# Kernel optimization log

Measured on AMD Instinct MI355X. Metric: run time of the kernel, lower is better.

## Reference

```python
import jax, jax.numpy as jnp
import numpy as np


def setup_inputs() -> dict:
    key = jax.random.key(0)
    k1, k2, k3, k4, k5 = jax.random.split(key, 5)
    B, S, IC, OC = 4, 2048, 4096, 4096
    n_out = int(0.05 * IC)  # 204 outlier columns
    return {
        "x": jax.random.normal(k1, (B, S, IC), dtype=jnp.float32),
        "weight": jax.random.normal(k2, (OC, IC), dtype=jnp.float32) * 0.02,
        "bias": jax.random.normal(k3, (OC,), dtype=jnp.float32) * 0.02,
        "outlier_weight": jax.random.normal(k4, (OC, n_out), dtype=jnp.float32) * 0.02,
        "outlier_columns_index": jax.random.randint(k5, (n_out,), 0, IC, dtype=jnp.int32),
    }


def reference(x, weight, bias, outlier_weight, outlier_columns_index):
    # XnorBinaryLinear.quant_weight: per-output-row mean-centering,
    # sign binarization, scaled by per-row mean absolute value.
    mean = jnp.mean(weight, axis=1, keepdims=True)            # [OC, 1]
    centered = weight - mean                                  # [OC, IC]
    scale = jnp.mean(jnp.abs(centered), axis=1, keepdims=True)  # [OC, 1]
    q = jnp.sign(centered) * scale                            # binarized weight [OC, IC]
    # scatter fp32 outlier columns back into the binarized weight
    w = q.at[:, outlier_columns_index].set(outlier_weight)    # [OC, IC]
    # F.linear(x, w, bias) = x @ w.T + bias
    out = jnp.einsum('bsi,oi->bso', x, w) + bias
    return out
```

## Files before the change

kernel.cpp:

```cpp
#include <hip/hip_runtime.h>
#include <hip/hip_bf16.h>


typedef __attribute__((ext_vector_type(4))) int i32x4;

__global__ void init_colmap_kernel(int* __restrict__ cm, int IC) {
    int i = blockIdx.x * 256 + threadIdx.x;
    if (i < IC) cm[i] = -1;
}

__global__ void scatter_colmap_kernel(const int* __restrict__ idx,
                                      int* __restrict__ cm, int n) {
    int j = blockIdx.x * 256 + threadIdx.x;
    if (j < n) atomicMax(&cm[idx[j]], j);
}

__global__ void quant_sign_kernel(const float* __restrict__ w,
                                  signed char* __restrict__ qw,
                                  float* __restrict__ sArr,
                                  float* __restrict__ meanArr,
                                  int IC, int K2) {
    __shared__ float red[8];
    const int o = blockIdx.x;
    const int t = threadIdx.x;
    const int lane = t & 63, wid = t >> 6;

    const float4* row4 = (const float4*)(w + (size_t)o * IC);
    float4 v[4];
    float s = 0.f;
#pragma unroll
    for (int j = 0; j < 4; ++j) {
        v[j] = row4[t + j * 256];
        s += v[j].x + v[j].y + v[j].z + v[j].w;
    }
#pragma unroll
    for (int off = 32; off; off >>= 1) s += __shfl_down(s, off);
    if (lane == 0) red[wid] = s;
    __syncthreads();
    const float mean = (red[0] + red[1] + red[2] + red[3]) / (float)IC;

    float a = 0.f;
#pragma unroll
    for (int j = 0; j < 4; ++j)
        a += fabsf(v[j].x - mean) + fabsf(v[j].y - mean) +
             fabsf(v[j].z - mean) + fabsf(v[j].w - mean);
#pragma unroll
    for (int off = 32; off; off >>= 1) a += __shfl_down(a, off);
    if (lane == 0) red[4 + wid] = a;
    __syncthreads();
    const float scale = (red[4] + red[5] + red[6] + red[7]) / (float)IC;

    if (t == 0) { sArr[o] = scale; meanArr[o] = mean; }

    const size_t base = (size_t)o * K2;
#pragma unroll
    for (int j = 0; j < 4; ++j) {
        const int c0 = (t + j * 256) * 4;
        float ee[4] = {v[j].x, v[j].y, v[j].z, v[j].w};
        int pack = 0;
#pragma unroll
        for (int ei = 0; ei < 4; ++ei) {
            float c = ee[ei] - mean;
            int q = c > 0.f ? 8 : (c < 0.f ? -8 : 0);
            pack |= (q & 0xff) << (ei * 8);
        }
        *(int*)(qw + base + c0) = pack;
    }
}

__global__ void corr_w_kernel(const float* __restrict__ w,
                              const float* __restrict__ ow,
                              const int* __restrict__ idx,
                              const int* __restrict__ cm,
                              const float* __restrict__ sArr,
                              const float* __restrict__ meanArr,
                              signed char* __restrict__ qw,
                              int IC, int K2, int n_out) {
    const int o = blockIdx.x;
    const int j = threadIdx.x;
    signed char q = 0;
    if (j < n_out) {
        const int c = idx[j];
        if (cm[c] == j) {
            const float s = sArr[o];
            const float cen = w[(size_t)o * IC + c] - meanArr[o];
            const float sg = cen > 0.f ? 1.f : (cen < 0.f ? -1.f : 0.f);
            const float wc = ow[(size_t)o * n_out + j] - s * sg;
            float qf = rintf(8.f * wc / s);
            qf = fminf(127.f, fmaxf(-127.f, qf));
            q = (signed char)(int)qf;
        }
    }
    qw[(size_t)o * K2 + IC + j] = q;
}

__global__ void quant_x_kernel(const float4* __restrict__ x4,
                               signed char* __restrict__ qx,
                               float* __restrict__ rdel,
                               int IC, int K2) {
    __shared__ float red[4];
    __shared__ float bmax;
    const int m = blockIdx.x;
    const int t = threadIdx.x;
    const int lane = t & 63, wid = t >> 6;

    const float4* row4 = x4 + (size_t)m * (IC / 4);
    float4 v[4];
    float mx = 0.f;
#pragma unroll
    for (int j = 0; j < 4; ++j) {
        v[j] = row4[t + j * 256];
        mx = fmaxf(mx, fmaxf(fmaxf(fabsf(v[j].x), fabsf(v[j].y)),
                             fmaxf(fabsf(v[j].z), fabsf(v[j].w))));
    }
#pragma unroll
    for (int off = 32; off; off >>= 1) mx = fmaxf(mx, __shfl_down(mx, off));
    if (lane == 0) red[wid] = mx;
    __syncthreads();
    if (t == 0) {
        float m0 = fmaxf(fmaxf(red[0], red[1]), fmaxf(red[2], red[3]));
        bmax = m0;
        rdel[m] = m0 / 127.f;
    }
    __syncthreads();
    const float inv = 127.f / bmax;

    const size_t base = (size_t)m * K2;
#pragma unroll
    for (int j = 0; j < 4; ++j) {
        const int c0 = (t + j * 256) * 4;
        float ee[4] = {v[j].x, v[j].y, v[j].z, v[j].w};
        int pack = 0;
#pragma unroll
        for (int ei = 0; ei < 4; ++ei) {
            int q = (int)rintf(ee[ei] * inv);
            pack |= (q & 0xff) << (ei * 8);
        }
        *(int*)(qx + base + c0) = pack;
    }
}

__global__ void gather_xo_kernel(signed char* __restrict__ qx,
                                 const int* __restrict__ idx,
                                 int IC, int K2, int n_out) {
    const int m = blockIdx.x;
    const int j = threadIdx.x;
    signed char v = 0;
    if (j < n_out) v = qx[(size_t)m * K2 + idx[j]];
    qx[(size_t)m * K2 + IC + j] = v;
}

#define GLDS(src, dst) __builtin_amdgcn_global_load_lds( \
    (const __attribute__((address_space(1))) void*)(src), \
    (__attribute__((address_space(3))) void*)(dst), 16, 0, 0)

#define STAGE64(MAT, bufS, knB) do {                                          \
    const signed char* gsrc_ = (MAT) ? Bblk : Ablk;                           \
    _Pragma("unroll")                                                         \
    for (int rr_ = 0; rr_ < 2; ++rr_) {                                       \
      GLDS(gsrc_ + (size_t)(rr_ * 128 + stg_row) * K2 + (knB) + stg_col,      \
           &ldsb[(bufS) * 32768 + (MAT) * 16384 + (rr_ * 128 + wid * 16) * 64]); \
    } } while (0)

#define RDA(AF, FH, B_) do {                                                  \
    const signed char* pa_ = &ldsb[(B_) * 32768];                             \
    _Pragma("unroll")                                                         \
    for (int j_ = 0; j_ < 4; ++j_)                                            \
      AF[j_] = *(const i32x4*)&pa_[(wr * 128 + ((FH) * 4 + j_) * 16 + l15) * 64 + slB]; \
  } while (0)

#define RDB(BF, B_) do {                                                      \
    const signed char* pb_ = &ldsb[(B_) * 32768 + 16384];                     \
    _Pragma("unroll")                                                         \
    for (int j_ = 0; j_ < 4; ++j_)                                            \
      BF[j_] = *(const i32x4*)&pb_[(wc * 64 + j_ * 16 + l15) * 64 + slB];     \
  } while (0)

#define MM16(FH) do {                                                         \
    _Pragma("unroll")                                                         \
    for (int mi_ = 0; mi_ < 4; ++mi_)                                         \
      _Pragma("unroll")                                                       \
      for (int ni_ = 0; ni_ < 4; ++ni_)                                       \
        acc[(FH) * 4 + mi_][ni_] = __builtin_amdgcn_mfma_i32_16x16x64_i8(     \
            afr[mi_], bfr[ni_], acc[(FH) * 4 + mi_][ni_], 0, 0, 0);           \
  } while (0)

#define PH64(FH, DOBF, STMAT, VM, bufR, bufS, knB) do {                       \
    if (DOBF) RDB(bfr, bufR);                                                 \
    RDA(afr, FH, bufR);                                                       \
    STAGE64(STMAT, bufS, knB);                                                \
    if (VM) asm volatile("s_waitcnt vmcnt(8)" ::: "memory");                  \
    __builtin_amdgcn_s_barrier();                                             \
    __builtin_amdgcn_s_setprio(1);                                            \
    MM16(FH);                                                                 \
    __builtin_amdgcn_s_setprio(0);                                            \
    __builtin_amdgcn_s_barrier();                                             \
  } while (0)

#define KT64(bufR, bufS, knB) do {                                            \
    PH64(0, true,  0, false, bufR, bufS, knB);                                \
    PH64(1, false, 1, true,  bufR, bufS, knB);                                \
  } while (0)

__global__ __launch_bounds__(512, 2) void gemm_i8_kernel(
    const signed char* __restrict__ Aq,
    const signed char* __restrict__ Bq,
    const float* __restrict__ bias,
    const float* __restrict__ sArr,
    const float* __restrict__ rdel,
    float* __restrict__ C,
    int M, int N, int K2, int NBN) {
    extern __shared__ signed char ldsb[];

    const int t = threadIdx.x;
    const int wid = t >> 6, lane = t & 63;
    const int l15 = lane & 15;
    const int slB = (((lane >> 4) ^ ((lane >> 1) & 3)) & 3) * 16;
    const int wr = wid >> 2;
    const int wc = wid & 3;
    const int stg_row = wid * 16 + (lane >> 2);
    const int stg_col = (((lane & 3) ^ ((lane >> 3) & 3)) & 3) * 16;

    const int nwg = gridDim.x;
    const int bid = blockIdx.x;
    const int q = nwg >> 3, r = nwg & 7;
    const int xcd = bid & 7, off = bid >> 3;
    const int swz = (xcd < r ? xcd * (q + 1) : r * (q + 1) + (xcd - r) * q) + off;
    const int bm = swz / NBN, bn = swz % NBN;

    const signed char* Ablk = Aq + (size_t)(bm * 256) * K2;
    const signed char* Bblk = Bq + (size_t)(bn * 256) * K2;

    i32x4 acc[8][4] = {};
    i32x4 afr[4], bfr[4];

    STAGE64(0, 0, 0);    STAGE64(1, 0, 0);
    STAGE64(0, 1, 64);   STAGE64(1, 1, 64);
    STAGE64(0, 2, 128);  STAGE64(1, 2, 128);
    asm volatile("s_waitcnt vmcnt(8)" ::: "memory");
    __builtin_amdgcn_s_barrier();

    for (int it = 0; it < 17; ++it) {
        const int tt = it * 4;
        const int k3 = (tt + 3) * 64;
        const int k4 = (tt + 4 < 68) ? (tt + 4) * 64 : 0;
        const int k5 = (tt + 5 < 68) ? (tt + 5) * 64 : 0;
        const int k6 = (tt + 6 < 68) ? (tt + 6) * 64 : 0;
        KT64(0, 3, k3);
        KT64(1, 0, k4);
        KT64(2, 1, k5);
        KT64(3, 2, k6);
    }

    float sv[4], bv[4];
#pragma unroll
    for (int ni = 0; ni < 4; ++ni) {
        const int col = bn * 256 + wc * 64 + ni * 16 + l15;
        sv[ni] = sArr[col] * 0.125f;
        bv[ni] = bias[col];
    }

    const int crow0 = bm * 256 + wr * 128;
    const int ccol = bn * 256 + wc * 64 + l15;
#pragma unroll
    for (int mi = 0; mi < 8; ++mi) {
#pragma unroll
        for (int rr = 0; rr < 4; ++rr) {
            const int row = crow0 + mi * 16 + (lane >> 4) * 4 + rr;
            const float rd = rdel[row];
            float* Crow = C + (size_t)row * N;
#pragma unroll
            for (int ni = 0; ni < 4; ++ni)
                Crow[ccol + ni * 16] =
                    (float)acc[mi][ni][rr] * (sv[ni] * rd) + bv[ni];
        }
    }
}

extern "C" void kernel_launch(void* const* d_in, const int* in_sizes, int n_in,
                              void* d_out, int out_size, void* d_ws, size_t ws_size,
                              hipStream_t stream) {
    const float* x      = (const float*)d_in[0];
    const float* weight = (const float*)d_in[1];
    const float* bias   = (const float*)d_in[2];
    const float* ow     = (const float*)d_in[3];
    const int*   idx    = (const int*)d_in[4];

    const int OC    = in_sizes[2];
    const int n_out = in_sizes[4];
    const int IC    = in_sizes[1] / OC;
    const int M     = in_sizes[0] / IC;
    const int K2    = IC + 256;
    float* out = (float*)d_out;

    char* ws = (char*)d_ws;
    signed char* qx = (signed char*)ws;
    signed char* qw = (signed char*)(ws + (size_t)M * K2);
    float* sArr   = (float*)(ws + (size_t)M * K2 + (size_t)OC * K2);
    float* meanArr= sArr + OC;
    float* rdel   = meanArr + OC;
    int*   cm     = (int*)(rdel + M);

    init_colmap_kernel<<<(IC + 255) / 256, 256, 0, stream>>>(cm, IC);
    scatter_colmap_kernel<<<(n_out + 255) / 256, 256, 0, stream>>>(idx, cm, n_out);
    quant_sign_kernel<<<OC, 256, 0, stream>>>(weight, qw, sArr, meanArr, IC, K2);
    corr_w_kernel<<<OC, 256, 0, stream>>>(weight, ow, idx, cm, sArr, meanArr,
                                          qw, IC, K2, n_out);
    quant_x_kernel<<<M, 256, 0, stream>>>((const float4*)x, qx, rdel, IC, K2);
    gather_xo_kernel<<<M, 256, 0, stream>>>(qx, idx, IC, K2, n_out);

    hipFuncSetAttribute((const void*)gemm_i8_kernel,
                        hipFuncAttributeMaxDynamicSharedMemorySize, 131072);
    const int NBM = M / 256, NBN = OC / 256;
    gemm_i8_kernel<<<dim3(NBM * NBN), dim3(512), 131072, stream>>>(
        qx, qw, bias, sArr, rdel, out, M, OC, K2, NBN);
}
```

Baseline: 202.7 us.

## Load GEMM A fragments straight from global memory and fuse outlier kernels

The int8 GEMM now stages only the weight (B) tile in LDS. Activation (A) fragments are read directly from global memory into registers, double-buffered across the two half-phases. This halves dynamic LDS to 64KB, so two workgroups can fit per CU, at the cost of redundant global/L2 reads of A across the four column waves. Separately, the outlier-column correction and activation gather are folded into the weight and activation quantization kernels using shared-memory copies, which removes two launches and their re-reads of global data.

```diff
diff --git a/kernel.cpp b/kernel.cpp
--- a/kernel.cpp
+++ b/kernel.cpp
@@ -16,11 +16,14 @@
 }
 
 __global__ void quant_sign_kernel(const float* __restrict__ w,
+                                  const float* __restrict__ ow,
+                                  const int* __restrict__ idx,
+                                  const int* __restrict__ cm,
                                   signed char* __restrict__ qw,
                                   float* __restrict__ sArr,
-                                  float* __restrict__ meanArr,
-                                  int IC, int K2) {
+                                  int IC, int K2, int n_out) {
     __shared__ float red[8];
+    __shared__ signed char sgn[4096];
     const int o = blockIdx.x;
     const int t = threadIdx.x;
     const int lane = t & 63, wid = t >> 6;
@@ -49,8 +52,7 @@
     if (lane == 0) red[4 + wid] = a;
     __syncthreads();
     const float scale = (red[4] + red[5] + red[6] + red[7]) / (float)IC;
-
-    if (t == 0) { sArr[o] = scale; meanArr[o] = mean; }
+    if (t == 0) sArr[o] = scale;
 
     const size_t base = (size_t)o * K2;
 #pragma unroll
@@ -65,41 +67,32 @@
             pack |= (q & 0xff) << (ei * 8);
         }
         *(int*)(qw + base + c0) = pack;
-    }
-}
-
-__global__ void corr_w_kernel(const float* __restrict__ w,
-                              const float* __restrict__ ow,
-                              const int* __restrict__ idx,
-                              const int* __restrict__ cm,
-                              const float* __restrict__ sArr,
-                              const float* __restrict__ meanArr,
-                              signed char* __restrict__ qw,
-                              int IC, int K2, int n_out) {
-    const int o = blockIdx.x;
-    const int j = threadIdx.x;
+        *(int*)(sgn + c0) = pack;
+    }
+    __syncthreads();
+
     signed char q = 0;
-    if (j < n_out) {
-        const int c = idx[j];
-        if (cm[c] == j) {
-            const float s = sArr[o];
-            const float cen = w[(size_t)o * IC + c] - meanArr[o];
-            const float sg = cen > 0.f ? 1.f : (cen < 0.f ? -1.f : 0.f);
-            const float wc = ow[(size_t)o * n_out + j] - s * sg;
-            float qf = rintf(8.f * wc / s);
+    if (t < n_out) {
+        const int c = idx[t];
+        if (cm[c] == t) {
+            const float sg = (float)sgn[c] * 0.125f;
+            const float wc = ow[(size_t)o * n_out + t] - scale * sg;
+            float qf = rintf(8.f * wc / scale);
             qf = fminf(127.f, fmaxf(-127.f, qf));
             q = (signed char)(int)qf;
         }
     }
-    qw[(size_t)o * K2 + IC + j] = q;
+    qw[base + IC + t] = q;
 }
 
 __global__ void quant_x_kernel(const float4* __restrict__ x4,
+                               const int* __restrict__ idx,
                                signed char* __restrict__ qx,
                                float* __restrict__ rdel,
-                               int IC, int K2) {
+                               int IC, int K2, int n_out) {
     __shared__ float red[4];
     __shared__ float bmax;
+    __shared__ signed char rowq[4096];
     const int m = blockIdx.x;
     const int t = threadIdx.x;
     const int lane = t & 63, wid = t >> 6;
@@ -137,69 +130,63 @@
             pack |= (q & 0xff) << (ei * 8);
         }
         *(int*)(qx + base + c0) = pack;
-    }
-}
-
-__global__ void gather_xo_kernel(signed char* __restrict__ qx,
-                                 const int* __restrict__ idx,
-                                 int IC, int K2, int n_out) {
-    const int m = blockIdx.x;
-    const int j = threadIdx.x;
-    signed char v = 0;
-    if (j < n_out) v = qx[(size_t)m * K2 + idx[j]];
-    qx[(size_t)m * K2 + IC + j] = v;
+        *(int*)(rowq + c0) = pack;
+    }
+    __syncthreads();
+
+    signed char g = 0;
+    if (t < n_out) g = rowq[idx[t]];
+    qx[base + IC + t] = g;
 }
 
 #define GLDS(src, dst) __builtin_amdgcn_global_load_lds( \
     (const __attribute__((address_space(1))) void*)(src), \
     (__attribute__((address_space(3))) void*)(dst), 16, 0, 0)
 
-#define STAGE64(MAT, bufS, knB) do {                                          \
-    const signed char* gsrc_ = (MAT) ? Bblk : Ablk;                           \
-    _Pragma("unroll")                                                         \
-    for (int rr_ = 0; rr_ < 2; ++rr_) {                                       \
-      GLDS(gsrc_ + (size_t)(rr_ * 128 + stg_row) * K2 + (knB) + stg_col,      \
-           &ldsb[(bufS) * 32768 + (MAT) * 16384 + (rr_ * 128 + wid * 16) * 64]); \
-    } } while (0)
-
-#define RDA(AF, FH, B_) do {                                                  \
-    const signed char* pa_ = &ldsb[(B_) * 32768];                             \
+#define STG(BUFS, KNB, RR) \
+    GLDS(Bblk + (size_t)((RR) * 128 + stg_row) * K2 + (KNB) + stg_col, \
+         &ldsb[(BUFS) * 16384 + ((RR) * 128 + wid * 16) * 64])
+
+#define RDB(B_) do {                                                          \
+    const signed char* pb_ = &ldsb[(B_) * 16384];                             \
     _Pragma("unroll")                                                         \
     for (int j_ = 0; j_ < 4; ++j_)                                            \
-      AF[j_] = *(const i32x4*)&pa_[(wr * 128 + ((FH) * 4 + j_) * 16 + l15) * 64 + slB]; \
+      bfr[j_] = *(const i32x4*)&pb_[(wc * 64 + j_ * 16 + l15) * 64 + slB];    \
   } while (0)
 
-#define RDB(BF, B_) do {                                                      \
-    const signed char* pb_ = &ldsb[(B_) * 32768 + 16384];                     \
+#define LDA4(DST, KADD, FH) do {                                              \
     _Pragma("unroll")                                                         \
     for (int j_ = 0; j_ < 4; ++j_)                                            \
-      BF[j_] = *(const i32x4*)&pb_[(wc * 64 + j_ * 16 + l15) * 64 + slB];     \
+      DST[j_] = *(const i32x4*)(aBase + (KADD) + aOff[(FH) * 4 + j_]);        \
   } while (0)
 
-#define MM16(FH) do {                                                         \
+#define MM16(AF, FH) do {                                                     \
     _Pragma("unroll")                                                         \
     for (int mi_ = 0; mi_ < 4; ++mi_)                                         \
       _Pragma("unroll")                                                       \
       for (int ni_ = 0; ni_ < 4; ++ni_)                                       \
         acc[(FH) * 4 + mi_][ni_] = __builtin_amdgcn_mfma_i32_16x16x64_i8(     \
-            afr[mi_], bfr[ni_], acc[(FH) * 4 + mi_][ni_], 0, 0, 0);           \
+            AF[mi_], bfr[ni_], acc[(FH) * 4 + mi_][ni_], 0, 0, 0);            \
   } while (0)
 
-#define PH64(FH, DOBF, STMAT, VM, bufR, bufS, knB) do {                       \
-    if (DOBF) RDB(bfr, bufR);                                                 \
-    RDA(afr, FH, bufR);                                                       \
-    STAGE64(STMAT, bufS, knB);                                                \
-    if (VM) asm volatile("s_waitcnt vmcnt(8)" ::: "memory");                  \
+#define KT(BUFR, BUFS, KNB) do {                                              \
+    RDB(BUFR);                                                                \
+    LDA4(afB, 0, 1);                                                          \
+    STG(BUFS, KNB, 0);                                                        \
     __builtin_amdgcn_s_barrier();                                             \
     __builtin_amdgcn_s_setprio(1);                                            \
-    MM16(FH);                                                                 \
+    MM16(afA, 0);                                                             \
     __builtin_amdgcn_s_setprio(0);                                            \
     __builtin_amdgcn_s_barrier();                                             \
-  } while (0)
-
-#define KT64(bufR, bufS, knB) do {                                            \
-    PH64(0, true,  0, false, bufR, bufS, knB);                                \
-    PH64(1, false, 1, true,  bufR, bufS, knB);                                \
+    LDA4(afA, 64, 0);                                                         \
+    STG(BUFS, KNB, 1);                                                        \
+    asm volatile("s_waitcnt vmcnt(6)" ::: "memory");                          \
+    __builtin_amdgcn_s_barrier();                                             \
+    __builtin_amdgcn_s_setprio(1);                                            \
+    MM16(afB, 1);                                                             \
+    __builtin_amdgcn_s_setprio(0);                                            \
+    __builtin_amdgcn_s_barrier();                                             \
+    aBase += 64;                                                              \
   } while (0)
 
 __global__ __launch_bounds__(512, 2) void gemm_i8_kernel(
@@ -228,28 +215,30 @@
     const int swz = (xcd < r ? xcd * (q + 1) : r * (q + 1) + (xcd - r) * q) + off;
     const int bm = swz / NBN, bn = swz % NBN;
 
-    const signed char* Ablk = Aq + (size_t)(bm * 256) * K2;
-    const signed char* Bblk = Bq + (size_t)(bn * 256) * K2;
+    const signed char* aBase = Aq + (size_t)(bm * 256) * K2;
+    const signed char* Bblk  = Bq + (size_t)(bn * 256) * K2;
+
+    int aOff[8];
+#pragma unroll
+    for (int f = 0; f < 8; ++f)
+        aOff[f] = (wr * 128 + f * 16 + l15) * K2 + (lane >> 4) * 16;
 
     i32x4 acc[8][4] = {};
-    i32x4 afr[4], bfr[4];
-
-    STAGE64(0, 0, 0);    STAGE64(1, 0, 0);
-    STAGE64(0, 1, 64);   STAGE64(1, 1, 64);
-    STAGE64(0, 2, 128);  STAGE64(1, 2, 128);
+    i32x4 afA[4], afB[4], bfr[4];
+
+    STG(0, 0, 0);    STG(0, 0, 1);
+    STG(1, 64, 0);   STG(1, 64, 1);
+    STG(2, 128, 0);  STG(2, 128, 1);
+    LDA4(afA, 0, 0);
     asm volatile("s_waitcnt vmcnt(8)" ::: "memory");
     __builtin_amdgcn_s_barrier();
 
     for (int it = 0; it < 17; ++it) {
-        const int tt = it * 4;
-        const int k3 = (tt + 3) * 64;
-        const int k4 = (tt + 4 < 68) ? (tt + 4) * 64 : 0;
-        const int k5 = (tt + 5 < 68) ? (tt + 5) * 64 : 0;
-        const int k6 = (tt + 6 < 68) ? (tt + 6) * 64 : 0;
-        KT64(0, 3, k3);
-        KT64(1, 0, k4);
-        KT64(2, 1, k5);
-        KT64(3, 2, k6);
+        const int kb = it * 256;
+        KT(0, 3, kb + 192);
+        KT(1, 0, kb + 256);
+        KT(2, 1, kb + 320);
+        KT(3, 2, kb + 384);
     }
 
     float sv[4], bv[4];
@@ -296,22 +285,20 @@
     char* ws = (char*)d_ws;
     signed char* qx = (signed char*)ws;
     signed char* qw = (signed char*)(ws + (size_t)M * K2);
-    float* sArr   = (float*)(ws + (size_t)M * K2 + (size_t)OC * K2);
-    float* meanArr= sArr + OC;
-    float* rdel   = meanArr + OC;
-    int*   cm     = (int*)(rdel + M);
+    float* sArr = (float*)(ws + (size_t)M * K2 + (size_t)OC * K2);
+    float* rdel = sArr + OC;
+    int*   cm   = (int*)(rdel + M);
 
     init_colmap_kernel<<<(IC + 255) / 256, 256, 0, stream>>>(cm, IC);
     scatter_colmap_kernel<<<(n_out + 255) / 256, 256, 0, stream>>>(idx, cm, n_out);
-    quant_sign_kernel<<<OC, 256, 0, stream>>>(weight, qw, sArr, meanArr, IC, K2);
-    corr_w_kernel<<<OC, 256, 0, stream>>>(weight, ow, idx, cm, sArr, meanArr,
-                                          qw, IC, K2, n_out);
-    quant_x_kernel<<<M, 256, 0, stream>>>((const float4*)x, qx, rdel, IC, K2);
-    gather_xo_kernel<<<M, 256, 0, stream>>>(qx, idx, IC, K2, n_out);
+    quant_sign_kernel<<<OC, 256, 0, stream>>>(weight, ow, idx, cm, qw, sArr,
+                                              IC, K2, n_out);
+    quant_x_kernel<<<M, 256, 0, stream>>>((const float4*)x, idx, qx, rdel,
+                                          IC, K2, n_out);
 
     hipFuncSetAttribute((const void*)gemm_i8_kernel,
-                        hipFuncAttributeMaxDynamicSharedMemorySize, 131072);
+                        hipFuncAttributeMaxDynamicSharedMemorySize, 65536);
     const int NBM = M / 256, NBN = OC / 256;
-    gemm_i8_kernel<<<dim3(NBM * NBN), dim3(512), 131072, stream>>>(
+    gemm_i8_kernel<<<dim3(NBM * NBN), dim3(512), 65536, stream>>>(
         qx, qw, bias, sArr, rdel, out, M, OC, K2, NBN);
 }
```

Measured after the change: 382.1 us. 88.5% more time.
